# Kernel optimization log

Hardware: AMD Instinct MI355X
Metric: run time of the kernel (lower is better)

Reference implementation:

```python
import jax, jax.numpy as jnp
import numpy as np

B, S, R, D_NODE, D_PAIR, N_HEAD, C = 1, 128, 256, 256, 128, 8, 32
EPS = 1e-5


def layer_norm(x, g, b):
    mu = jnp.mean(x, axis=-1, keepdims=True)
    var = jnp.mean(jnp.square(x - mu), axis=-1, keepdims=True)
    return (x - mu) * jax.lax.rsqrt(var + EPS) * g + b


def self_attention(x, qkv_w, qkv_b, gate_w, gate_b, o_w, o_b, bias=None):
    # x: [B, n1, n2, d]; attends over n2. heads: n_head x c, n_head*c == d.
    b_, n1, n2, d = x.shape
    qkv = x @ qkv_w.T + qkv_b                      # [B, n1, n2, 3*h*c]
    q, k, v = jnp.split(qkv, 3, axis=-1)
    split_heads = lambda t: t.reshape(b_, n1, n2, N_HEAD, C).transpose(0, 1, 3, 2, 4)  # [B,n1,h,n2,c]
    q = split_heads(q) * (C ** -0.5)
    k = split_heads(k)
    v = split_heads(v)
    logits = jnp.einsum('bshqc,bshkc->bshqk', q, k)  # [B, n1, h, n2, n2]
    if bias is not None:
        logits = logits + bias[:, None]              # bias: [B, h, n2, n2]
    w = jax.nn.softmax(logits, axis=-1)
    o = jnp.einsum('bshqk,bshkc->bshqc', w, v)
    o = o.transpose(0, 1, 3, 2, 4).reshape(b_, n1, n2, N_HEAD * C)
    gate = jax.nn.sigmoid(x @ gate_w.T + gate_b)
    o = o * gate
    out = o @ o_w.T
    if o_b is not None:
        out = out + o_b
    return out


def setup_inputs() -> dict:
    key = jax.random.key(0)
    ks = jax.random.split(key, 12)
    rn = lambda k, sh, sc=1.0: jax.random.normal(k, sh, dtype=jnp.float32) * sc
    return {
        'node': rn(ks[0], (B, S, R, D_NODE)),
        'pair': rn(ks[1], (B, R, R, D_PAIR)),
        'ln_mr_g': jnp.ones((D_NODE,), jnp.float32), 'ln_mr_b': jnp.zeros((D_NODE,), jnp.float32),
        'ln_z_g': jnp.ones((D_PAIR,), jnp.float32), 'ln_z_b': jnp.zeros((D_PAIR,), jnp.float32),
        'b_weights': rn(ks[2], (N_HEAD, D_PAIR), D_PAIR ** -0.5),
        'row_qkv_w': rn(ks[3], (3 * N_HEAD * C, D_NODE), D_NODE ** -0.5),
        'row_qkv_b': jnp.zeros((3 * N_HEAD * C,), jnp.float32),
        'row_gate_w': rn(ks[4], (N_HEAD * C, D_NODE), D_NODE ** -0.5),
        'row_gate_b': jnp.ones((N_HEAD * C,), jnp.float32),
        'row_o_w': rn(ks[5], (D_NODE, N_HEAD * C), D_NODE ** -0.5),
        'out_bias': jnp.zeros((D_NODE,), jnp.float32),
        'ln_mc_g': jnp.ones((D_NODE,), jnp.float32), 'ln_mc_b': jnp.zeros((D_NODE,), jnp.float32),
        'col_qkv_w': rn(ks[6], (3 * N_HEAD * C, D_NODE), D_NODE ** -0.5),
        'col_qkv_b': jnp.zeros((3 * N_HEAD * C,), jnp.float32),
        'col_gate_w': rn(ks[7], (N_HEAD * C, D_NODE), D_NODE ** -0.5),
        'col_gate_b': jnp.ones((N_HEAD * C,), jnp.float32),
        'col_o_w': rn(ks[8], (D_NODE, N_HEAD * C), D_NODE ** -0.5),
        'col_o_b': jnp.zeros((D_NODE,), jnp.float32),
        'ln_t_g': jnp.ones((D_NODE,), jnp.float32), 'ln_t_b': jnp.zeros((D_NODE,), jnp.float32),
        't_w1': rn(ks[9], (4 * D_NODE, D_NODE), D_NODE ** -0.5),
        't_b1': jnp.zeros((4 * D_NODE,), jnp.float32),
        't_w2': rn(ks[10], (D_NODE, 4 * D_NODE), (4 * D_NODE) ** -0.5),
        't_b2': jnp.zeros((D_NODE,), jnp.float32),
    }


def reference(node, pair, ln_mr_g, ln_mr_b, ln_z_g, ln_z_b, b_weights,
              row_qkv_w, row_qkv_b, row_gate_w, row_gate_b, row_o_w, out_bias,
              ln_mc_g, ln_mc_b, col_qkv_w, col_qkv_b, col_gate_w, col_gate_b, col_o_w, col_o_b,
              ln_t_g, ln_t_b, t_w1, t_b1, t_w2, t_b2):
    # --- MSARowAttentionWithPairBias ---
    M = layer_norm(node, ln_mr_g, ln_mr_b)                 # [B,S,R,D]
    Z = layer_norm(pair, ln_z_g, ln_z_b)                   # [B,R,R,Dp]
    b = jnp.einsum('bqkd,hd->bhqk', Z, b_weights)          # pair bias [B,h,R,R]
    M = self_attention(M, row_qkv_w, row_qkv_b, row_gate_w, row_gate_b, row_o_w, None, bias=b)
    # bias_dropout_add with ones dropout mask (inference): residual + (x + bias)
    node = node + M + out_bias
    # --- MSAColumnAttention ---
    Mt = node.transpose(0, 2, 1, 3)                        # [B,R,S,D], attend over S
    Mt = layer_norm(Mt, ln_mc_g, ln_mc_b)
    Mt = self_attention(Mt, col_qkv_w, col_qkv_b, col_gate_w, col_gate_b, col_o_w, col_o_b)
    node = node + Mt.transpose(0, 2, 1, 3)
    # --- MSATransition (n=4) ---
    x = layer_norm(node, ln_t_g, ln_t_b)
    x = jax.nn.relu(x @ t_w1.T + t_b1) @ t_w2.T + t_b2
    return node + x
```

## Files before the change

kernel.cpp:

```cpp
#include <hip/hip_runtime.h>
#include <hip/hip_bf16.h>

#define EPS 1e-5f

typedef __hip_bfloat16 bf16;
typedef __attribute__((ext_vector_type(8))) short short8v;
typedef __attribute__((ext_vector_type(4))) short short4v;
typedef __attribute__((ext_vector_type(4))) float f32x4;

__device__ inline f32x4 mfma16bf(short4v a, short4v b, f32x4 c) {
#if __has_builtin(__builtin_amdgcn_mfma_f32_16x16x16bf16_1k)
  return __builtin_amdgcn_mfma_f32_16x16x16bf16_1k(a, b, c, 0, 0, 0);
#else
  short8v a8 = {a[0], a[1], a[2], a[3], 0, 0, 0, 0};
  short8v b8 = {b[0], b[1], b[2], b[3], 0, 0, 0, 0};
  return __builtin_amdgcn_mfma_f32_16x16x32_bf16(a8, b8, c, 0, 0, 0);
#endif
}

__device__ inline void load_lds16(const void* g, void* l) {
  __builtin_amdgcn_global_load_lds(
      (const __attribute__((address_space(1))) void*)g,
      (__attribute__((address_space(3))) void*)l, 16, 0, 0);
}

__device__ inline unsigned pack_bf16x2(float a, float b) {
  union { bf16 h[2]; unsigned u; } cv;
  cv.h[0] = __float2bfloat16(a);
  cv.h[1] = __float2bfloat16(b);
  return cv.u;
}

#define QSCALE 0.17677669529663687f

struct CvtArgs {
  const float* src[8];
  bf16* dst[8];
  int n4[8];
  int scale_n4[8];
};

__global__ __launch_bounds__(256) void cvt_all_kernel(CvtArgs a) {
  int i = blockIdx.x * 256 + threadIdx.x;
#pragma unroll
  for (int s = 0; s < 8; ++s) {
    if (i < a.n4[s]) {
      float4 v = reinterpret_cast<const float4*>(a.src[s])[i];
      float sc = (i < a.scale_n4[s]) ? QSCALE : 1.0f;
      union { ushort4 u; bf16 h[4]; } cv;
      cv.h[0] = __float2bfloat16(v.x * sc);
      cv.h[1] = __float2bfloat16(v.y * sc);
      cv.h[2] = __float2bfloat16(v.z * sc);
      cv.h[3] = __float2bfloat16(v.w * sc);
      reinterpret_cast<ushort4*>(a.dst[s])[i] = cv.u;
      return;
    }
    i -= a.n4[s];
  }
}

__global__ __launch_bounds__(256) void bias_concat_kernel(
    const float* rq, const float* rg, const float* cq, const float* cg,
    float* br, float* bc) {
  int i = blockIdx.x * 256 + threadIdx.x;
  if (i < 1024) {
    float v = (i < 768) ? rq[i] : rg[i - 768];
    br[i] = (i < 256) ? v * QSCALE : v;
  } else {
    int j = i - 1024;
    float v = (j < 768) ? cq[j] : cg[j - 768];
    bc[j] = (j < 256) ? v * QSCALE : v;
  }
}

__global__ __launch_bounds__(512) void ln256_bf_kernel(
    const float* __restrict__ in, bf16* __restrict__ out,
    const float* __restrict__ g, const float* __restrict__ b) {
  int tid = threadIdx.x;
  int w = tid >> 6, lane = tid & 63;
  int row0 = blockIdx.x * 16 + w * 2;
  const float4* r0 = reinterpret_cast<const float4*>(in + (size_t)row0 * 256);
  const float4* r1 =
      reinterpret_cast<const float4*>(in + (size_t)(row0 + 1) * 256);
  float4 x0 = r0[lane];
  float4 x1 = r1[lane];
  float4 gv = reinterpret_cast<const float4*>(g)[lane];
  float4 bv = reinterpret_cast<const float4*>(b)[lane];

  float s0 = x0.x + x0.y + x0.z + x0.w;
  float q0 = x0.x * x0.x + x0.y * x0.y + x0.z * x0.z + x0.w * x0.w;
  float s1 = x1.x + x1.y + x1.z + x1.w;
  float q1 = x1.x * x1.x + x1.y * x1.y + x1.z * x1.z + x1.w * x1.w;
#pragma unroll
  for (int off = 32; off >= 1; off >>= 1) {
    s0 += __shfl_xor(s0, off);
    q0 += __shfl_xor(q0, off);
    s1 += __shfl_xor(s1, off);
    q1 += __shfl_xor(q1, off);
  }
  float m0 = s0 * (1.0f / 256.0f);
  float i0 = rsqrtf(q0 * (1.0f / 256.0f) - m0 * m0 + EPS);
  float m1 = s1 * (1.0f / 256.0f);
  float i1 = rsqrtf(q1 * (1.0f / 256.0f) - m1 * m1 + EPS);

  union { ushort4 u; bf16 h[4]; } c0, c1;
  c0.h[0] = __float2bfloat16((x0.x - m0) * i0 * gv.x + bv.x);
  c0.h[1] = __float2bfloat16((x0.y - m0) * i0 * gv.y + bv.y);
  c0.h[2] = __float2bfloat16((x0.z - m0) * i0 * gv.z + bv.z);
  c0.h[3] = __float2bfloat16((x0.w - m0) * i0 * gv.w + bv.w);
  c1.h[0] = __float2bfloat16((x1.x - m1) * i1 * gv.x + bv.x);
  c1.h[1] = __float2bfloat16((x1.y - m1) * i1 * gv.y + bv.y);
  c1.h[2] = __float2bfloat16((x1.z - m1) * i1 * gv.z + bv.z);
  c1.h[3] = __float2bfloat16((x1.w - m1) * i1 * gv.w + bv.w);
  reinterpret_cast<ushort4*>(out + (size_t)row0 * 256)[lane] = c0.u;
  reinterpret_cast<ushort4*>(out + (size_t)(row0 + 1) * 256)[lane] = c1.u;
}

__global__ __launch_bounds__(256) void pair_bias_kernel(
    const float* __restrict__ pair, const float* __restrict__ g,
    const float* __restrict__ b, const float* __restrict__ bw,
    float* __restrict__ bT) {
  int tid = threadIdx.x;
  int w = tid >> 6, lane = tid & 63;
  int l15 = lane & 15, l4 = lane >> 4;
  int rowbase = blockIdx.x * 64 + w * 16;
  const float* zrow = pair + (size_t)(rowbase + l15) * 128;

  float z[4][8];
#pragma unroll
  for (int kk = 0; kk < 4; ++kk) {
    float4 a0 = *reinterpret_cast<const float4*>(zrow + kk * 32 + l4 * 8);
    float4 a1 = *reinterpret_cast<const float4*>(zrow + kk * 32 + l4 * 8 + 4);
    z[kk][0] = a0.x; z[kk][1] = a0.y; z[kk][2] = a0.z; z[kk][3] = a0.w;
    z[kk][4] = a1.x; z[kk][5] = a1.y; z[kk][6] = a1.z; z[kk][7] = a1.w;
  }
  float s = 0.0f, sq = 0.0f;
#pragma unroll
  for (int kk = 0; kk < 4; ++kk)
#pragma unroll
    for (int e = 0; e < 8; ++e) {
      s += z[kk][e];
      sq += z[kk][e] * z[kk][e];
    }
  s += __shfl_xor(s, 16);
  s += __shfl_xor(s, 32);
  sq += __shfl_xor(sq, 16);
  sq += __shfl_xor(sq, 32);
  float mu = s * (1.0f / 128.0f);
  float inv = rsqrtf(sq * (1.0f / 128.0f) - mu * mu + EPS);

  f32x4 acc = {0.f, 0.f, 0.f, 0.f};
#pragma unroll
  for (int kk = 0; kk < 4; ++kk) {
    const float* gp = g + kk * 32 + l4 * 8;
    const float* bp = b + kk * 32 + l4 * 8;
    float4 g0 = *reinterpret_cast<const float4*>(gp);
    float4 g1 = *reinterpret_cast<const float4*>(gp + 4);
    float4 b0 = *reinterpret_cast<const float4*>(bp);
    float4 b1 = *reinterpret_cast<const float4*>(bp + 4);
    float gv[8] = {g0.x, g0.y, g0.z, g0.w, g1.x, g1.y, g1.z, g1.w};
    float bv[8] = {b0.x, b0.y, b0.z, b0.w, b1.x, b1.y, b1.z, b1.w};
    union { short8v v; bf16 h[8]; } af;
#pragma unroll
    for (int e = 0; e < 8; ++e)
      af.h[e] = __float2bfloat16((z[kk][e] - mu) * inv * gv[e] + bv[e]);
    union { short8v v; bf16 h[8]; } bwf;
    if (l15 < 8) {
      const float* wp = bw + l15 * 128 + kk * 32 + l4 * 8;
      float4 w0 = *reinterpret_cast<const float4*>(wp);
      float4 w1 = *reinterpret_cast<const float4*>(wp + 4);
      float wv[8] = {w0.x, w0.y, w0.z, w0.w, w1.x, w1.y, w1.z, w1.w};
#pragma unroll
      for (int e = 0; e < 8; ++e) bwf.h[e] = __float2bfloat16(wv[e]);
    } else {
      bwf.v = short8v{0, 0, 0, 0, 0, 0, 0, 0};
    }
    acc = __builtin_amdgcn_mfma_f32_16x16x32_bf16(af.v, bwf.v, acc, 0, 0, 0);
  }
  if (l15 < 8) {
#pragma unroll
    for (int r = 0; r < 4; ++r)
      bT[(size_t)l15 * 65536 + rowbase + l4 * 4 + r] = acc[r];
  }
}

template <int EPI, int AMAP, int OMAP>
__global__ __launch_bounds__(256) void gemm_mfma_kernel(
    const bf16* __restrict__ A, const bf16* __restrict__ W,
    const float* __restrict__ bias, const float* __restrict__ aux, void* out,
    int N, int K, int nbn) {
  __shared__ __align__(16) short As[2][128 * 32];
  __shared__ __align__(16) short Bs[2][128 * 32];
  int nwg = gridDim.x;
  int qch = nwg >> 3;
  int flat = blockIdx.x;
  int wg = (flat & 7) * qch + (flat >> 3);
  int bm = wg / nbn, bn = wg % nbn;
  int tid = threadIdx.x;
  int w = tid >> 6, lane = tid & 63;
  int wr = w >> 1, wc = w & 1;
  int c0 = w * 64 + lane;
  int srow = c0 >> 2, skq = c0 & 3;
  const short* Aptr = (const short*)A;
  const short* Wbase = (const short*)(W + (size_t)(bn * 128) * K);
  f32x4 acc[4][4] = {};
  int lrow = lane & 15, kq = lane >> 4;

  auto arow = [&](int r) -> size_t {
    return AMAP ? ((size_t)r * 256 + bm) : ((size_t)(bm * 128 + r));
  };
  auto stage = [&](int buf, int k0) {
    load_lds16(Aptr + arow(srow) * K + k0 + skq * 8, &As[buf][c0 * 8]);
    load_lds16(Aptr + arow(srow + 64) * K + k0 + skq * 8,
               &As[buf][(256 + c0) * 8]);
    load_lds16(Wbase + (size_t)srow * K + k0 + skq * 8, &Bs[buf][c0 * 8]);
    load_lds16(Wbase + (size_t)(srow + 64) * K + k0 + skq * 8,
               &Bs[buf][(256 + c0) * 8]);
  };

  stage(0, 0);
  __syncthreads();
  int nk = K >> 5;
  for (int t = 0; t < nk; ++t) {
    int cur = t & 1;
    if (t + 1 < nk) stage(cur ^ 1, (t + 1) << 5);
    short8v af[4], bfv[4];
#pragma unroll
    for (int i = 0; i < 4; ++i)
      af[i] = *reinterpret_cast<const short8v*>(
          &As[cur][(wr * 64 + i * 16 + lrow) * 32 + kq * 8]);
#pragma unroll
    for (int j = 0; j < 4; ++j)
      bfv[j] = *reinterpret_cast<const short8v*>(
          &Bs[cur][(wc * 64 + j * 16 + lrow) * 32 + kq * 8]);
#pragma unroll
    for (int i = 0; i < 4; ++i)
#pragma unroll
      for (int j = 0; j < 4; ++j)
        acc[i][j] = __builtin_amdgcn_mfma_f32_16x16x32_bf16(af[i], bfv[j],
                                                            acc[i][j], 0, 0, 0);
    __syncthreads();
  }

  float* outF = (float*)out;
  bf16* outB = (bf16*)out;
  int r4 = (lane >> 4) * 4;
#pragma unroll
  for (int j = 0; j < 4; ++j) {
    int c = bn * 128 + wc * 64 + j * 16 + lrow;
    float bv = bias ? bias[c] : 0.0f;
#pragma unroll
    for (int i = 0; i < 4; ++i) {
      int lr0 = wr * 64 + i * 16 + r4;
#pragma unroll
      for (int reg = 0; reg < 4; ++reg) {
        int lr = lr0 + reg;
        size_t off = OMAP ? (((size_t)lr * 256 + bm) * N + c)
                          : ((size_t)(bm * 128 + lr) * N + c);
        float v = acc[i][j][reg] + bv;
        if (EPI == 0) {
          outB[off] = __float2bfloat16(v);
        } else if (EPI == 2) {
          outF[off] = v + aux[off];
        } else {
          outB[off] = __float2bfloat16(fmaxf(v, 0.0f));
        }
      }
    }
  }
}

template <bool ROWMODE>
__global__ __launch_bounds__(512) void attn_mfma_kernel(
    const bf16* __restrict__ qkv, const float* __restrict__ bT,
    bf16* __restrict__ o) {
  constexpr int KVLEN = ROWMODE ? 256 : 128;
  constexpr int QT = ROWMODE ? 2 : 1;
  constexpr int KOUT = KVLEN / 64;
  constexpr int STRIDE = 1024;
  constexpr int NT = 512;
  __shared__ __align__(16) short K_lds[KVLEN * 32];
  __shared__ __align__(16) short Vt_lds[32 * KVLEN];

  int b = blockIdx.x;
  int idx = b >> 3, h = b & 7;
  const short* qb = (const short*)qkv + (size_t)idx * (KVLEN * 1024);
  const bf16* qbh = (const bf16*)qb;
  bf16* ob = o + (size_t)idx * (KVLEN * 256);
  int tid = threadIdx.x;
  int w = tid >> 6, lane = tid & 63;
  int l15 = lane & 15, l4 = lane >> 4;

#pragma unroll
  for (int rnd = 0; rnd < (KVLEN * 4) / NT; ++rnd) {
    int c = rnd * NT + tid;
    int row = c >> 2;
    int kq = (c & 3) ^ ((row >> 1) & 3);
    load_lds16(qb + (size_t)row * STRIDE + 256 + h * 32 + kq * 8,
               &K_lds[c * 8]);
  }
  {
    int tt = tid;
    if (KVLEN * 2 == NT || tt < KVLEN * 2) {
      int kp = tt >> 2;
      int cc = (tt & 3) * 8;
      short8v va = *reinterpret_cast<const short8v*>(
          qb + (size_t)(2 * kp) * STRIDE + 512 + h * 32 + cc);
      short8v vb = *reinterpret_cast<const short8v*>(
          qb + (size_t)(2 * kp + 1) * STRIDE + 512 + h * 32 + cc);
      int k = 2 * kp;
      int u = k >> 3;
      int klo = k & 7;
#pragma unroll
      for (int e = 0; e < 8; ++e) {
        int cI = cc + e;
        int up = u ^ (cI & 7);
        unsigned pk = (unsigned)(unsigned short)va[e] |
                      ((unsigned)(unsigned short)vb[e] << 16);
        *reinterpret_cast<unsigned*>(&Vt_lds[cI * KVLEN + up * 8 + klo]) = pk;
      }
    }
  }
  __syncthreads();

  int q0 = w * QT * 16;
  short8v qf[QT];
#pragma unroll
  for (int j = 0; j < QT; ++j)
    qf[j] = *reinterpret_cast<const short8v*>(
        qb + (size_t)(q0 + j * 16 + l15) * STRIDE + h * 32 + l4 * 8);

  f32x4 acc_o[QT][2] = {};
  f32x4 acc_l[QT] = {};
  const short4v ones = {0x3F80, 0x3F80, 0x3F80, 0x3F80};

  const float L2E = 1.4426950408889634f;
  const f32x4 zf = {0.f, 0.f, 0.f, 0.f};

#pragma unroll 1
  for (int kt = 0; kt < KOUT; ++kt) {
    float4 bb[QT][4];
    if (ROWMODE) {
#pragma unroll
      for (int j = 0; j < QT; ++j) {
        const float* bq = bT + (size_t)h * 65536 +
                          (size_t)(q0 + j * 16 + l15) * 256 + kt * 64 + l4 * 4;
#pragma unroll
        for (int i = 0; i < 4; ++i)
          bb[j][i] = *reinterpret_cast<const float4*>(bq + i * 16);
      }
    }
    short8v kf[4];
#pragma unroll
    for (int i = 0; i < 4; ++i) {
      int krow = kt * 64 + i * 16 + l15;
      kf[i] = *reinterpret_cast<const short8v*>(
          &K_lds[krow * 32 + ((l4 ^ ((krow >> 1) & 3)) * 8)]);
    }
    short4v vfa[4][2];
#pragma unroll
    for (int ks4 = 0; ks4 < 4; ++ks4)
#pragma unroll
      for (int ct = 0; ct < 2; ++ct) {
        int cI = ct * 16 + l15;
        int u = kt * 8 + ks4 * 2 + (l4 >> 1);
        vfa[ks4][ct] = *reinterpret_cast<const short4v*>(
            &Vt_lds[cI * KVLEN + (u ^ (cI & 7)) * 8 + (l4 & 1) * 4]);
      }

#pragma unroll
    for (int j = 0; j < QT; ++j) {
      f32x4 accs[4];
#pragma unroll
      for (int i = 0; i < 4; ++i) {
        f32x4 cin = zf;
        if (ROWMODE) {
          cin[0] = bb[j][i].x;
          cin[1] = bb[j][i].y;
          cin[2] = bb[j][i].z;
          cin[3] = bb[j][i].w;
        }
        accs[i] =
            __builtin_amdgcn_mfma_f32_16x16x32_bf16(kf[i], qf[j], cin, 0, 0, 0);
      }
#pragma unroll
      for (int i = 0; i < 4; ++i)
#pragma unroll
        for (int r = 0; r < 4; ++r)
          accs[i][r] = exp2f(accs[i][r] * L2E);
#pragma unroll
      for (int ks4 = 0; ks4 < 4; ++ks4) {
        union { unsigned u2[2]; short4v s; } pb;
        pb.u2[0] = pack_bf16x2(accs[ks4][0], accs[ks4][1]);
        pb.u2[1] = pack_bf16x2(accs[ks4][2], accs[ks4][3]);
#pragma unroll
        for (int ct = 0; ct < 2; ++ct)
          acc_o[j][ct] = mfma16bf(vfa[ks4][ct], pb.s, acc_o[j][ct]);
        acc_l[j] = mfma16bf(ones, pb.s, acc_l[j]);
      }
    }
  }

#pragma unroll
  for (int j = 0; j < QT; ++j) {
    float inv = 1.0f / acc_l[j][0];
    int row = q0 + j * 16 + l15;
    const bf16* grow = qbh + (size_t)row * STRIDE + 768 + h * 32;
    bf16* orow = ob + (size_t)row * 256 + h * 32;
#pragma unroll
    for (int ct = 0; ct < 2; ++ct) {
      int cc = ct * 16 + l4 * 4;
      ushort4 gv = *reinterpret_cast<const ushort4*>(grow + cc);
      union { ushort4 u; bf16 h4[4]; } gu, ou;
      gu.u = gv;
#pragma unroll
      for (int r = 0; r < 4; ++r) {
        float gt = __bfloat162float(gu.h4[r]);
        float sg = 1.0f / (1.0f + __expf(-gt));
        ou.h4[r] = __float2bfloat16(acc_o[j][ct][r] * inv * sg);
      }
      *reinterpret_cast<ushort4*>(orow + cc) = ou.u;
    }
  }
}

extern "C" void kernel_launch(void* const* d_in, const int* in_sizes, int n_in,
                              void* d_out, int out_size, void* d_ws,
                              size_t ws_size, hipStream_t stream) {
  (void)in_sizes; (void)n_in; (void)out_size; (void)ws_size;
  const float* node      = (const float*)d_in[0];
  const float* pair      = (const float*)d_in[1];
  const float* ln_mr_g   = (const float*)d_in[2];
  const float* ln_mr_b   = (const float*)d_in[3];
  const float* ln_z_g    = (const float*)d_in[4];
  const float* ln_z_b    = (const float*)d_in[5];
  const float* b_weights = (const float*)d_in[6];
  const float* row_qkv_w = (const float*)d_in[7];
  const float* row_qkv_b = (const float*)d_in[8];
  const float* row_gate_w= (const float*)d_in[9];
  const float* row_gate_b= (const float*)d_in[10];
  const float* row_o_w   = (const float*)d_in[11];
  const float* out_bias  = (const float*)d_in[12];
  const float* ln_mc_g   = (const float*)d_in[13];
  const float* ln_mc_b   = (const float*)d_in[14];
  const float* col_qkv_w = (const float*)d_in[15];
  const float* col_qkv_b = (const float*)d_in[16];
  const float* col_gate_w= (const float*)d_in[17];
  const float* col_gate_b= (const float*)d_in[18];
  const float* col_o_w   = (const float*)d_in[19];
  const float* col_o_b   = (const float*)d_in[20];
  const float* ln_t_g    = (const float*)d_in[21];
  const float* ln_t_b    = (const float*)d_in[22];
  const float* t_w1      = (const float*)d_in[23];
  const float* t_b1      = (const float*)d_in[24];
  const float* t_w2      = (const float*)d_in[25];
  const float* t_b2      = (const float*)d_in[26];
  float* out = (float*)d_out;

  const size_t NR = 32768;
  char* p = (char*)d_ws;
  float* buf_node = (float*)p; p += NR * 256 * 4;
  char*  qkv_region = p;       p += NR * 1024 * 2;
  float* buf_bias = (float*)p; p += 8 * 256 * 256 * 4;
  bf16* ln_bf     = (bf16*)p;  p += NR * 256 * 2;
  bf16* g_bf      = (bf16*)p;  p += NR * 256 * 2;
  bf16* qkv_bf = (bf16*)qkv_region;
  bf16* h_bf   = (bf16*)qkv_region;
  bf16* w_rqkvg = (bf16*)p; p += 1024 * 256 * 2;
  bf16* w_ro    = (bf16*)p; p += 256 * 256 * 2;
  bf16* w_cqkvg = (bf16*)p; p += 1024 * 256 * 2;
  bf16* w_co    = (bf16*)p; p += 256 * 256 * 2;
  bf16* w_t1    = (bf16*)p; p += 1024 * 256 * 2;
  bf16* w_t2    = (bf16*)p; p += 256 * 1024 * 2;
  float* b_rqkvg = (float*)p; p += 1024 * 4;
  float* b_cqkvg = (float*)p; p += 1024 * 4;

  CvtArgs ca;
  ca.src[0] = row_qkv_w;  ca.dst[0] = w_rqkvg;             ca.n4[0] = 49152;
  ca.src[1] = row_gate_w; ca.dst[1] = w_rqkvg + 768 * 256; ca.n4[1] = 16384;
  ca.src[2] = row_o_w;    ca.dst[2] = w_ro;                ca.n4[2] = 16384;
  ca.src[3] = col_qkv_w;  ca.dst[3] = w_cqkvg;             ca.n4[3] = 49152;
  ca.src[4] = col_gate_w; ca.dst[4] = w_cqkvg + 768 * 256; ca.n4[4] = 16384;
  ca.src[5] = col_o_w;    ca.dst[5] = w_co;                ca.n4[5] = 16384;
  ca.src[6] = t_w1;       ca.dst[6] = w_t1;                ca.n4[6] = 65536;
  ca.src[7] = t_w2;       ca.dst[7] = w_t2;                ca.n4[7] = 65536;
  for (int s = 0; s < 8; ++s) ca.scale_n4[s] = 0;
  ca.scale_n4[0] = 16384;
  ca.scale_n4[3] = 16384;
  cvt_all_kernel<<<1152, 256, 0, stream>>>(ca);
  bias_concat_kernel<<<8, 256, 0, stream>>>(row_qkv_b, row_gate_b, col_qkv_b,
                                            col_gate_b, b_rqkvg, b_cqkvg);

  ln256_bf_kernel<<<2048, 512, 0, stream>>>(node, ln_bf, ln_mr_g, ln_mr_b);
  pair_bias_kernel<<<1024, 256, 0, stream>>>(pair, ln_z_g, ln_z_b, b_weights,
                                             buf_bias);
  gemm_mfma_kernel<0, 0, 0><<<2048, 256, 0, stream>>>(
      ln_bf, w_rqkvg, b_rqkvg, nullptr, qkv_bf, 1024, 256, 8);
  attn_mfma_kernel<true><<<1024, 512, 0, stream>>>(qkv_bf, buf_bias, g_bf);
  gemm_mfma_kernel<2, 0, 0><<<512, 256, 0, stream>>>(
      g_bf, w_ro, out_bias, node, buf_node, 256, 256, 2);

  ln256_bf_kernel<<<2048, 512, 0, stream>>>(buf_node, ln_bf, ln_mc_g, ln_mc_b);
  gemm_mfma_kernel<0, 1, 0><<<2048, 256, 0, stream>>>(
      ln_bf, w_cqkvg, b_cqkvg, nullptr, qkv_bf, 1024, 256, 8);
  attn_mfma_kernel<false><<<2048, 512, 0, stream>>>(qkv_bf, nullptr, g_bf);
  gemm_mfma_kernel<2, 0, 1><<<512, 256, 0, stream>>>(
      g_bf, w_co, col_o_b, buf_node, buf_node, 256, 256, 2);

  ln256_bf_kernel<<<2048, 512, 0, stream>>>(buf_node, ln_bf, ln_t_g, ln_t_b);
  gemm_mfma_kernel<3, 0, 0><<<2048, 256, 0, stream>>>(
      ln_bf, w_t1, t_b1, nullptr, h_bf, 1024, 256, 8);
  gemm_mfma_kernel<2, 0, 0><<<512, 256, 0, stream>>>(
      h_bf, w_t2, t_b2, buf_node, out, 256, 1024, 2);
}
```

Measured before the change: 303.2 us.

## Software-pipeline attention QK/exp/PV stages and vectorize GEMM epilogue stores

The attention inner loop is restructured so that the QK MFMA for the next tile and the bias loads are issued before the PV MFMA of the previous tile. This lets exp and MFMA work overlap instead of running as serial dependent phases. The GEMM swaps its MFMA operand order so each lane holds four consecutive output columns, which turns the epilogue bias reads, aux reads and stores into 4-wide vector accesses. The pair-bias kernel also writes its result as float4. The software pipeline adds register pressure and macro-based control flow.

```diff
diff --git a/kernel.cpp b/kernel.cpp
--- a/kernel.cpp
+++ b/kernel.cpp
@@ -79,11 +79,9 @@
   int tid = threadIdx.x;
   int w = tid >> 6, lane = tid & 63;
   int row0 = blockIdx.x * 16 + w * 2;
-  const float4* r0 = reinterpret_cast<const float4*>(in + (size_t)row0 * 256);
-  const float4* r1 =
-      reinterpret_cast<const float4*>(in + (size_t)(row0 + 1) * 256);
-  float4 x0 = r0[lane];
-  float4 x1 = r1[lane];
+  float4 x0 = reinterpret_cast<const float4*>(in + (size_t)row0 * 256)[lane];
+  float4 x1 =
+      reinterpret_cast<const float4*>(in + (size_t)(row0 + 1) * 256)[lane];
   float4 gv = reinterpret_cast<const float4*>(g)[lane];
   float4 bv = reinterpret_cast<const float4*>(b)[lane];
 
@@ -178,9 +176,9 @@
     acc = __builtin_amdgcn_mfma_f32_16x16x32_bf16(af.v, bwf.v, acc, 0, 0, 0);
   }
   if (l15 < 8) {
-#pragma unroll
-    for (int r = 0; r < 4; ++r)
-      bT[(size_t)l15 * 65536 + rowbase + l4 * 4 + r] = acc[r];
+    float4 o4 = make_float4(acc[0], acc[1], acc[2], acc[3]);
+    *reinterpret_cast<float4*>(&bT[(size_t)l15 * 65536 + rowbase + l4 * 4]) =
+        o4;
   }
 }
 
@@ -237,34 +235,45 @@
     for (int i = 0; i < 4; ++i)
 #pragma unroll
       for (int j = 0; j < 4; ++j)
-        acc[i][j] = __builtin_amdgcn_mfma_f32_16x16x32_bf16(af[i], bfv[j],
+        acc[i][j] = __builtin_amdgcn_mfma_f32_16x16x32_bf16(bfv[j], af[i],
                                                             acc[i][j], 0, 0, 0);
     __syncthreads();
   }
 
   float* outF = (float*)out;
   bf16* outB = (bf16*)out;
-  int r4 = (lane >> 4) * 4;
 #pragma unroll
   for (int j = 0; j < 4; ++j) {
-    int c = bn * 128 + wc * 64 + j * 16 + lrow;
-    float bv = bias ? bias[c] : 0.0f;
+    int cc = bn * 128 + wc * 64 + j * 16 + kq * 4;
+    float4 bv4 = bias ? *reinterpret_cast<const float4*>(bias + cc)
+                      : make_float4(0.f, 0.f, 0.f, 0.f);
 #pragma unroll
     for (int i = 0; i < 4; ++i) {
-      int lr0 = wr * 64 + i * 16 + r4;
-#pragma unroll
-      for (int reg = 0; reg < 4; ++reg) {
-        int lr = lr0 + reg;
-        size_t off = OMAP ? (((size_t)lr * 256 + bm) * N + c)
-                          : ((size_t)(bm * 128 + lr) * N + c);
-        float v = acc[i][j][reg] + bv;
-        if (EPI == 0) {
-          outB[off] = __float2bfloat16(v);
-        } else if (EPI == 2) {
-          outF[off] = v + aux[off];
-        } else {
-          outB[off] = __float2bfloat16(fmaxf(v, 0.0f));
-        }
+      int lr = wr * 64 + i * 16 + lrow;
+      size_t off = OMAP ? (((size_t)lr * 256 + bm) * N + cc)
+                        : ((size_t)(bm * 128 + lr) * N + cc);
+      float v0 = acc[i][j][0] + bv4.x;
+      float v1 = acc[i][j][1] + bv4.y;
+      float v2 = acc[i][j][2] + bv4.z;
+      float v3 = acc[i][j][3] + bv4.w;
+      if (EPI == 0) {
+        union { ushort4 u; bf16 h[4]; } cv;
+        cv.h[0] = __float2bfloat16(v0);
+        cv.h[1] = __float2bfloat16(v1);
+        cv.h[2] = __float2bfloat16(v2);
+        cv.h[3] = __float2bfloat16(v3);
+        *reinterpret_cast<ushort4*>(outB + off) = cv.u;
+      } else if (EPI == 2) {
+        float4 av = *reinterpret_cast<const float4*>(aux + off);
+        *reinterpret_cast<float4*>(outF + off) =
+            make_float4(v0 + av.x, v1 + av.y, v2 + av.z, v3 + av.w);
+      } else {
+        union { ushort4 u; bf16 h[4]; } cv;
+        cv.h[0] = __float2bfloat16(fmaxf(v0, 0.0f));
+        cv.h[1] = __float2bfloat16(fmaxf(v1, 0.0f));
+        cv.h[2] = __float2bfloat16(fmaxf(v2, 0.0f));
+        cv.h[3] = __float2bfloat16(fmaxf(v3, 0.0f));
+        *reinterpret_cast<ushort4*>(outB + off) = cv.u;
       }
     }
   }
@@ -333,73 +342,100 @@
   f32x4 acc_o[QT][2] = {};
   f32x4 acc_l[QT] = {};
   const short4v ones = {0x3F80, 0x3F80, 0x3F80, 0x3F80};
-
   const float L2E = 1.4426950408889634f;
   const f32x4 zf = {0.f, 0.f, 0.f, 0.f};
 
+  f32x4 accs[4];
+  short4v P[4];
+  float4 bb0[4], bb1[4];
+
+#define LOAD_BIAS(KT, JJ, BB)                                               \
+  if (ROWMODE) {                                                            \
+    const float* bq_ = bT + (size_t)h * 65536 +                             \
+                       (size_t)(q0 + (JJ) * 16 + l15) * 256 + (KT) * 64 +   \
+                       l4 * 4;                                              \
+    _Pragma("unroll") for (int i_ = 0; i_ < 4; ++i_) BB[i_] =               \
+        *reinterpret_cast<const float4*>(bq_ + i_ * 16);                    \
+  }
+
+#define DO_QK(KT, JJ, BB)                                                   \
+  {                                                                         \
+    _Pragma("unroll") for (int i_ = 0; i_ < 4; ++i_) {                      \
+      int krow_ = (KT) * 64 + i_ * 16 + l15;                                \
+      short8v kf_ = *reinterpret_cast<const short8v*>(                      \
+          &K_lds[krow_ * 32 + ((l4 ^ ((krow_ >> 1) & 3)) * 8)]);            \
+      f32x4 cin_ = zf;                                                      \
+      if (ROWMODE) {                                                        \
+        cin_[0] = BB[i_].x; cin_[1] = BB[i_].y;                             \
+        cin_[2] = BB[i_].z; cin_[3] = BB[i_].w;                             \
+      }                                                                     \
+      accs[i_] = __builtin_amdgcn_mfma_f32_16x16x32_bf16(kf_, qf[JJ], cin_, \
+                                                         0, 0, 0);          \
+    }                                                                       \
+  }
+
+#define DO_EXPPACK()                                                        \
+  {                                                                         \
+    _Pragma("unroll") for (int i_ = 0; i_ < 4; ++i_) {                      \
+      float t0_ = exp2f(accs[i_][0] * L2E);                                 \
+      float t1_ = exp2f(accs[i_][1] * L2E);                                 \
+      float t2_ = exp2f(accs[i_][2] * L2E);                                 \
+      float t3_ = exp2f(accs[i_][3] * L2E);                                 \
+      union { unsigned u2[2]; short4v s; } pb_;                             \
+      pb_.u2[0] = pack_bf16x2(t0_, t1_);                                    \
+      pb_.u2[1] = pack_bf16x2(t2_, t3_);                                    \
+      P[i_] = pb_.s;                                                        \
+    }                                                                       \
+  }
+
+#define DO_PV(KT, JJ)                                                       \
+  {                                                                         \
+    _Pragma("unroll") for (int ks_ = 0; ks_ < 4; ++ks_) {                   \
+      _Pragma("unroll") for (int ct_ = 0; ct_ < 2; ++ct_) {                 \
+        int cI_ = ct_ * 16 + l15;                                           \
+        int u_ = (KT) * 8 + ks_ * 2 + (l4 >> 1);                            \
+        short4v vf_ = *reinterpret_cast<const short4v*>(                    \
+            &Vt_lds[cI_ * KVLEN + (u_ ^ (cI_ & 7)) * 8 + (l4 & 1) * 4]);    \
+        acc_o[JJ][ct_] = mfma16bf(vf_, P[ks_], acc_o[JJ][ct_]);             \
+      }                                                                     \
+      acc_l[JJ] = mfma16bf(ones, P[ks_], acc_l[JJ]);                        \
+    }                                                                       \
+  }
+
+  if constexpr (QT == 2) {
+    LOAD_BIAS(0, 0, bb0);
+    DO_QK(0, 0, bb0);
+    LOAD_BIAS(0, 1, bb1);
+    DO_EXPPACK();
 #pragma unroll 1
-  for (int kt = 0; kt < KOUT; ++kt) {
-    float4 bb[QT][4];
-    if (ROWMODE) {
-#pragma unroll
-      for (int j = 0; j < QT; ++j) {
-        const float* bq = bT + (size_t)h * 65536 +
-                          (size_t)(q0 + j * 16 + l15) * 256 + kt * 64 + l4 * 4;
-#pragma unroll
-        for (int i = 0; i < 4; ++i)
-          bb[j][i] = *reinterpret_cast<const float4*>(bq + i * 16);
+    for (int kt = 0; kt < KOUT; ++kt) {
+      DO_QK(kt, 1, bb1);
+      if (kt + 1 < KOUT) LOAD_BIAS(kt + 1, 0, bb0);
+      DO_PV(kt, 0);
+      DO_EXPPACK();
+      if (kt + 1 < KOUT) {
+        DO_QK(kt + 1, 0, bb0);
+        LOAD_BIAS(kt + 1, 1, bb1);
+        DO_PV(kt, 1);
+        DO_EXPPACK();
       }
     }
-    short8v kf[4];
-#pragma unroll
-    for (int i = 0; i < 4; ++i) {
-      int krow = kt * 64 + i * 16 + l15;
-      kf[i] = *reinterpret_cast<const short8v*>(
-          &K_lds[krow * 32 + ((l4 ^ ((krow >> 1) & 3)) * 8)]);
-    }
-    short4v vfa[4][2];
-#pragma unroll
-    for (int ks4 = 0; ks4 < 4; ++ks4)
-#pragma unroll
-      for (int ct = 0; ct < 2; ++ct) {
-        int cI = ct * 16 + l15;
-        int u = kt * 8 + ks4 * 2 + (l4 >> 1);
-        vfa[ks4][ct] = *reinterpret_cast<const short4v*>(
-            &Vt_lds[cI * KVLEN + (u ^ (cI & 7)) * 8 + (l4 & 1) * 4]);
-      }
-
-#pragma unroll
-    for (int j = 0; j < QT; ++j) {
-      f32x4 accs[4];
-#pragma unroll
-      for (int i = 0; i < 4; ++i) {
-        f32x4 cin = zf;
-        if (ROWMODE) {
-          cin[0] = bb[j][i].x;
-          cin[1] = bb[j][i].y;
-          cin[2] = bb[j][i].z;
-          cin[3] = bb[j][i].w;
-        }
-        accs[i] =
-            __builtin_amdgcn_mfma_f32_16x16x32_bf16(kf[i], qf[j], cin, 0, 0, 0);
-      }
-#pragma unroll
-      for (int i = 0; i < 4; ++i)
-#pragma unroll
-        for (int r = 0; r < 4; ++r)
-          accs[i][r] = exp2f(accs[i][r] * L2E);
-#pragma unroll
-      for (int ks4 = 0; ks4 < 4; ++ks4) {
-        union { unsigned u2[2]; short4v s; } pb;
-        pb.u2[0] = pack_bf16x2(accs[ks4][0], accs[ks4][1]);
-        pb.u2[1] = pack_bf16x2(accs[ks4][2], accs[ks4][3]);
-#pragma unroll
-        for (int ct = 0; ct < 2; ++ct)
-          acc_o[j][ct] = mfma16bf(vfa[ks4][ct], pb.s, acc_o[j][ct]);
-        acc_l[j] = mfma16bf(ones, pb.s, acc_l[j]);
-      }
-    }
-  }
+    DO_PV(KOUT - 1, 1);
+  } else {
+    DO_QK(0, 0, bb0);
+    DO_EXPPACK();
+#pragma unroll 1
+    for (int kt = 1; kt < KOUT; ++kt) {
+      DO_QK(kt, 0, bb0);
+      DO_PV(kt - 1, 0);
+      DO_EXPPACK();
+    }
+    DO_PV(KOUT - 1, 0);
+  }
+#undef LOAD_BIAS
+#undef DO_QK
+#undef DO_EXPPACK
+#undef DO_PV
 
 #pragma unroll
   for (int j = 0; j < QT; ++j) {
```

Measured after the change: 300.1 us. Within noise of the previous version (-1.0%).
